# Optimization experiments

Measured on AMD Instinct MI355X. Metric: run time of the kernel, lower is better.

Reference implementation:

```python
import jax, jax.numpy as jnp
import numpy as np

B, S, D = 8, 2048, 512  # batch, seq_len, d_model (= units*heads = 64*8)


def setup_inputs() -> dict:
    key = jax.random.key(0)
    k1, k2, k3, k4 = jax.random.split(key, 4)
    scale = 1.0 / np.sqrt(D)
    return {
        "data": jax.random.normal(k1, (B, S, D), dtype=jnp.float32),
        "Wq": jax.random.normal(k2, (D, D), dtype=jnp.float32) * scale,
        "Wk": jax.random.normal(k3, (D, D), dtype=jnp.float32) * scale,
        "Wv": jax.random.normal(k4, (D, D), dtype=jnp.float32) * scale,
    }


def reference(data, Wq, Wk, Wv):
    # Bias-free projections (no head split in the original module).
    q = data @ Wq  # [B,S,D]
    k = data @ Wk
    v = data @ Wv
    scores = jnp.einsum("bsd,btd->bst", q, k)  # [B,S,S]
    # NOTE: original scales by sqrt(weight.shape[-1]) == sqrt(seq_len), not sqrt(d_k).
    scores = scores / jnp.sqrt(jnp.float32(scores.shape[-1]))
    # Causal mask: (w + 1e6) * tril - 1e6  ==  where(tril, w, -1e6)
    causal = jnp.tril(jnp.ones((scores.shape[1], scores.shape[2]), dtype=bool))
    scores = jnp.where(causal[None, :, :], scores, jnp.float32(-1e6))
    attn = jax.nn.softmax(scores, axis=-1)
    return jnp.einsum("bst,btd->bsd", attn, v)  # [B,S,D]
```

## Files before the change

### kernel.cpp

```cpp
#include <hip/hip_runtime.h>

typedef unsigned short u16;
typedef __attribute__((ext_vector_type(8))) short short8;
typedef __attribute__((ext_vector_type(4))) float f32x4;


__device__ __forceinline__ u16 f2bf(float f) {
    unsigned u = __float_as_uint(f);
    u += 0x7fffu + ((u >> 16) & 1u);
    return (u16)(u >> 16);
}

__device__ __forceinline__ void lds_cp16(const u16* g, u16* l) {
#if defined(__has_builtin) && __has_builtin(__builtin_amdgcn_global_load_lds)
    __builtin_amdgcn_global_load_lds(
        (const __attribute__((address_space(1))) void*)g,
        (__attribute__((address_space(3))) void*)l, 16, 0, 0);
#else
    *(uint4*)l = *(const uint4*)g;
#endif
}

__device__ __forceinline__ void skew(int bid) {
    const int slot = bid >> 8;
    for (int i = 0; i < slot; ++i) __builtin_amdgcn_s_sleep(7);
}

template <int MI, bool ROWSUM>
__device__ __forceinline__ void gemm64(const u16* __restrict__ Ag, int lda,
                                       const u16* __restrict__ Bg, int ldb,
                                       int ksteps, u16* Alds, u16* Blds,
                                       f32x4 (&acc)[MI][4], f32x4* accL) {
    const int t = threadIdx.x;
    const int lane = t & 63, w = t >> 6;
    const int l15 = lane & 15, g4 = lane >> 4;
    const int wr = (w >> 1) * (MI * 16);
    const int wc = (w & 1) * 64;
    const int swz = l15 & 7;
    const short ob = (short)0x3f80;
    const short8 ones = {ob, ob, ob, ob, ob, ob, ob, ob};

    for (int kt = 0; kt < ksteps; ++kt) {
        __syncthreads();
#pragma unroll
        for (int p = 0; p < MI; ++p) {
            const int gi = t + p * 256;
            const int row = gi >> 3;
            const int gl = (gi & 7) ^ (row & 7);
            lds_cp16(Ag + (size_t)row * lda + kt * 64 + gl * 8, Alds + gi * 8);
        }
#pragma unroll
        for (int p = 0; p < 4; ++p) {
            const int gi = t + p * 256;
            const int row = gi >> 3;
            const int gl = (gi & 7) ^ (row & 7);
            lds_cp16(Bg + (size_t)row * ldb + kt * 64 + gl * 8, Blds + gi * 8);
        }
        __syncthreads();
#pragma unroll
        for (int ks = 0; ks < 2; ++ks) {
            short8 a[MI], b[4];
#pragma unroll
            for (int i = 0; i < MI; ++i) {
                const int r = wr + i * 16 + l15;
                a[i] = *(const short8*)(Alds + r * 64 + (((ks * 4 + g4) ^ swz) * 8));
            }
#pragma unroll
            for (int j = 0; j < 4; ++j) {
                const int r = wc + j * 16 + l15;
                b[j] = *(const short8*)(Blds + r * 64 + (((ks * 4 + g4) ^ swz) * 8));
            }
#pragma unroll
            for (int i = 0; i < MI; ++i)
#pragma unroll
                for (int j = 0; j < 4; ++j)
                    acc[i][j] = __builtin_amdgcn_mfma_f32_16x16x32_bf16(a[i], b[j], acc[i][j], 0, 0, 0);
            if constexpr (ROWSUM) {
#pragma unroll
                for (int i = 0; i < MI; ++i)
                    accL[i] = __builtin_amdgcn_mfma_f32_16x16x32_bf16(a[i], ones, accL[i], 0, 0, 0);
            }
        }
    }
}


__global__ void k_cvt(const float4* __restrict__ X4, ushort4* __restrict__ Xb4,
                      const float* __restrict__ Wq, const float* __restrict__ Wk,
                      const float* __restrict__ Wv, u16* __restrict__ Wt) {
    const int bid = blockIdx.x, t = threadIdx.x;
    if (bid < 2048) {
        const int n4 = (8 * 2048 * 512) / 4;
        for (int i = bid * 256 + t; i < n4; i += 2048 * 256) {
            float4 v = X4[i];
            ushort4 o;
            o.x = f2bf(v.x); o.y = f2bf(v.y); o.z = f2bf(v.z); o.w = f2bf(v.w);
            Xb4[i] = o;
        }
    } else {
        const int e0 = ((bid - 2048) * 256 + t) * 4;
#pragma unroll
        for (int p = 0; p < 4; ++p) {
            const int idx = e0 + p;
            const int z = idx >> 18;
            const int rem = idx & 262143;
            float v;
            if (z == 0) v = Wq[rem];
            else if (z == 1) v = Wk[rem];
            else { int n = rem >> 9, k = rem & 511; v = Wv[k * 512 + n]; }
            Wt[idx] = f2bf(v);
        }
    }
}

__global__ __launch_bounds__(256, 4) void k_gemm_m(const u16* __restrict__ Wt, u16* __restrict__ Mt) {
    __shared__ alignas(16) u16 Alds[8192];
    __shared__ alignas(16) u16 Blds[8192];
    const int mt = blockIdx.x & 3, nt = blockIdx.x >> 2;
    const u16* Ag = Wt + 0 * 512 * 512 + (size_t)mt * 128 * 512;
    const u16* Bg = Wt + 1 * 512 * 512 + (size_t)nt * 128 * 512;
    f32x4 acc[4][4] = {};
    gemm64<4, false>(Ag, 512, Bg, 512, 8, Alds, Blds, acc, (f32x4*)nullptr);

    const int t = threadIdx.x, lane = t & 63, w = t >> 6;
    const int wr = (w >> 1) * 64, wc = (w & 1) * 64;
    const float sc = 0.022097086912079608f;
#pragma unroll
    for (int i = 0; i < 4; ++i)
#pragma unroll
        for (int j = 0; j < 4; ++j)
#pragma unroll
            for (int r = 0; r < 4; ++r) {
                int e = mt * 128 + wr + i * 16 + 4 * (lane >> 4) + r;
                int f = nt * 128 + wc + j * 16 + (lane & 15);
                Mt[(size_t)f * 512 + e] = f2bf(acc[i][j][r] * sc);
            }
}

__global__ __launch_bounds__(256, 4) void k_proj(const u16* __restrict__ Xb, const u16* __restrict__ Wt,
                                                 const u16* __restrict__ Mt,
                                                 u16* __restrict__ Gb, u16* __restrict__ Vt) {
    __shared__ alignas(16) u16 Alds[8192];
    __shared__ alignas(16) u16 Blds[8192];
    const int bid = blockIdx.x;
    const int u = bid >> 3;
    const int z = u >> 6;
    const int nt = (u >> 4) & 3;
    const int mt = (bid & 7) * 16 + (u & 15);
    const u16* Ag = Xb + (size_t)mt * 128 * 512;
    const u16* Bg = (z == 0) ? (Mt + (size_t)nt * 128 * 512)
                             : (Wt + 2 * 512 * 512 + (size_t)nt * 128 * 512);
    skew(bid);
    f32x4 acc[4][4] = {};
    gemm64<4, false>(Ag, 512, Bg, 512, 8, Alds, Blds, acc, (f32x4*)nullptr);

    const int t = threadIdx.x, lane = t & 63, w = t >> 6;
    const int wr = (w >> 1) * 64, wc = (w & 1) * 64;
    if (z == 0) {
#pragma unroll
        for (int i = 0; i < 4; ++i)
#pragma unroll
            for (int j = 0; j < 4; ++j)
#pragma unroll
                for (int r = 0; r < 4; ++r) {
                    int m = mt * 128 + wr + i * 16 + 4 * (lane >> 4) + r;
                    int n = nt * 128 + wc + j * 16 + (lane & 15);
                    Gb[(size_t)m * 512 + n] = f2bf(acc[i][j][r]);
                }
    } else {
        int b = mt >> 4;
#pragma unroll
        for (int i = 0; i < 4; ++i)
#pragma unroll
            for (int j = 0; j < 4; ++j) {
                int s0 = (mt * 128 + wr + i * 16 + 4 * (lane >> 4)) & 2047;
                int d = nt * 128 + wc + j * 16 + (lane & 15);
                ushort4 pk;
                pk.x = f2bf(acc[i][j][0]); pk.y = f2bf(acc[i][j][1]);
                pk.z = f2bf(acc[i][j][2]); pk.w = f2bf(acc[i][j][3]);
                *(ushort4*)(Vt + (size_t)b * 512 * 2048 + (size_t)d * 2048 + s0) = pk;
            }
    }
}

__global__ __launch_bounds__(256, 4) void k_scores(const u16* __restrict__ Gb, const u16* __restrict__ Xb,
                                                   u16* __restrict__ P) {
    const int bid = blockIdx.x;
    const int bz = bid & 7;
    const int tt = bid >> 3;
    int qi = (int)((sqrtf(8.0f * tt + 1.0f) - 1.0f) * 0.5f);
    while ((qi + 1) * (qi + 2) / 2 <= tt) ++qi;
    while (qi * (qi + 1) / 2 > tt) --qi;
    const int kvj = tt - qi * (qi + 1) / 2;

    __shared__ alignas(16) u16 Alds[8192];
    __shared__ alignas(16) u16 Blds[8192];
    const u16* Ag = Gb + (size_t)bz * 2048 * 512 + (size_t)qi * 128 * 512;
    const u16* Bg = Xb + (size_t)bz * 2048 * 512 + (size_t)kvj * 128 * 512;
    skew(bid);
    f32x4 acc[4][4] = {};
    gemm64<4, false>(Ag, 512, Bg, 512, 8, Alds, Blds, acc, (f32x4*)nullptr);

    const int t = threadIdx.x, lane = t & 63, w = t >> 6;
    const int wr = (w >> 1) * 64, wc = (w & 1) * 64;
    u16* Pb = P + (size_t)bz * 2048 * 2048;
#pragma unroll
    for (int i = 0; i < 4; ++i)
#pragma unroll
        for (int j = 0; j < 4; ++j)
#pragma unroll
            for (int r = 0; r < 4; ++r) {
                int q = qi * 128 + wr + i * 16 + 4 * (lane >> 4) + r;
                int kv = kvj * 128 + wc + j * 16 + (lane & 15);
                float pv = (kv <= q) ? __expf(acc[i][j][r]) : 0.0f;
                Pb[(size_t)q * 2048 + kv] = f2bf(pv);
            }
}

__global__ __launch_bounds__(256, 4) void k_pv(const u16* __restrict__ P, const u16* __restrict__ Vt,
                                               float* __restrict__ Out) {
    __shared__ alignas(16) u16 Alds[4096];
    __shared__ alignas(16) u16 Blds[8192];
    const int bid = blockIdx.x;
    const int bz = bid & 7;
    const int u = bid >> 3;
    const int g = u >> 5;
    const int s = u & 31;
    const int nt = g;
    const int qi2 = (g & 1) ? (31 - s) : s;
    const int ksteps = qi2 + 1;

    const u16* Ag = P + (size_t)bz * 2048 * 2048 + (size_t)qi2 * 64 * 2048;
    const u16* Bg = Vt + (size_t)bz * 512 * 2048 + (size_t)nt * 128 * 2048;
    skew(bid);
    f32x4 acc[2][4] = {};
    f32x4 accL[2] = {};
    gemm64<2, true>(Ag, 2048, Bg, 2048, ksteps, Alds, Blds, acc, accL);

    const int t = threadIdx.x, lane = t & 63, w = t >> 6;
    const int l = lane & 15, g4 = lane >> 4;
    const int wr = (w >> 1) * 32, wc = (w & 1) * 64;
#pragma unroll
    for (int i = 0; i < 2; ++i) {
        float inv[4];
#pragma unroll
        for (int r = 0; r < 4; ++r) inv[r] = 1.0f / accL[i][r];
#pragma unroll
        for (int j = 0; j < 4; ++j) {
            const int d = nt * 128 + wc + j * 16 + l;
#pragma unroll
            for (int r = 0; r < 4; ++r) {
                const int q = qi2 * 64 + wr + i * 16 + 4 * g4 + r;
                Out[(size_t)bz * 2048 * 512 + (size_t)q * 512 + d] = acc[i][j][r] * inv[r];
            }
        }
    }
}


extern "C" void kernel_launch(void* const* d_in, const int* in_sizes, int n_in,
                              void* d_out, int out_size, void* d_ws, size_t ws_size,
                              hipStream_t stream) {
    const float* data = (const float*)d_in[0];
    const float* Wq = (const float*)d_in[1];
    const float* Wk = (const float*)d_in[2];
    const float* Wv = (const float*)d_in[3];
    float* out = (float*)d_out;
    char* ws = (char*)d_ws;

    u16* Xb = (u16*)(ws);
    u16* Gb = (u16*)(ws + 16777216);
    u16* Mt = (u16*)(ws + 33554432);
    u16* Vt = (u16*)(ws + 50331648);
    u16* Wt = (u16*)(ws + 67108864);
    u16* P  = (u16*)(ws + 68681728);

    k_cvt<<<2816, 256, 0, stream>>>((const float4*)data, (ushort4*)Xb, Wq, Wk, Wv, Wt);
    k_gemm_m<<<16, 256, 0, stream>>>(Wt, Mt);
    k_proj<<<1024, 256, 0, stream>>>(Xb, Wt, Mt, Gb, Vt);
    k_scores<<<1088, 256, 0, stream>>>(Gb, Xb, P);
    k_pv<<<1024, 256, 0, stream>>>(P, Vt, out);
}
```

Before: 111.0 us.

## Use 512-thread blocks with larger tiles for projection, scores and PV kernels

Result: slower. 119.2 us (+7.3%).

```diff
diff --git a/kernel.cpp b/kernel.cpp
--- a/kernel.cpp
+++ b/kernel.cpp
@@ -21,11 +21,6 @@
 #endif
 }
 
-__device__ __forceinline__ void skew(int bid) {
-    const int slot = bid >> 8;
-    for (int i = 0; i < slot; ++i) __builtin_amdgcn_s_sleep(7);
-}
-
 template <int MI, bool ROWSUM>
 __device__ __forceinline__ void gemm64(const u16* __restrict__ Ag, int lda,
                                        const u16* __restrict__ Bg, int ldb,
@@ -52,6 +47,64 @@
 #pragma unroll
         for (int p = 0; p < 4; ++p) {
             const int gi = t + p * 256;
+            const int row = gi >> 3;
+            const int gl = (gi & 7) ^ (row & 7);
+            lds_cp16(Bg + (size_t)row * ldb + kt * 64 + gl * 8, Blds + gi * 8);
+        }
+        __syncthreads();
+#pragma unroll
+        for (int ks = 0; ks < 2; ++ks) {
+            short8 a[MI], b[4];
+#pragma unroll
+            for (int i = 0; i < MI; ++i) {
+                const int r = wr + i * 16 + l15;
+                a[i] = *(const short8*)(Alds + r * 64 + (((ks * 4 + g4) ^ swz) * 8));
+            }
+#pragma unroll
+            for (int j = 0; j < 4; ++j) {
+                const int r = wc + j * 16 + l15;
+                b[j] = *(const short8*)(Blds + r * 64 + (((ks * 4 + g4) ^ swz) * 8));
+            }
+#pragma unroll
+            for (int i = 0; i < MI; ++i)
+#pragma unroll
+                for (int j = 0; j < 4; ++j)
+                    acc[i][j] = __builtin_amdgcn_mfma_f32_16x16x32_bf16(a[i], b[j], acc[i][j], 0, 0, 0);
+            if constexpr (ROWSUM) {
+#pragma unroll
+                for (int i = 0; i < MI; ++i)
+                    accL[i] = __builtin_amdgcn_mfma_f32_16x16x32_bf16(a[i], ones, accL[i], 0, 0, 0);
+            }
+        }
+    }
+}
+
+template <int MI, bool ROWSUM>
+__device__ __forceinline__ void gemm512(const u16* __restrict__ Ag, int lda,
+                                        const u16* __restrict__ Bg, int ldb,
+                                        int ksteps, u16* Alds, u16* Blds,
+                                        f32x4 (&acc)[MI][4], f32x4* accL) {
+    const int t = threadIdx.x;
+    const int lane = t & 63, w = t >> 6;
+    const int l15 = lane & 15, g4 = lane >> 4;
+    const int wr = (w >> 1) * (MI * 16);
+    const int wc = (w & 1) * 64;
+    const int swz = l15 & 7;
+    const short ob = (short)0x3f80;
+    const short8 ones = {ob, ob, ob, ob, ob, ob, ob, ob};
+
+    for (int kt = 0; kt < ksteps; ++kt) {
+        __syncthreads();
+#pragma unroll
+        for (int p = 0; p < MI; ++p) {
+            const int gi = t + p * 512;
+            const int row = gi >> 3;
+            const int gl = (gi & 7) ^ (row & 7);
+            lds_cp16(Ag + (size_t)row * lda + kt * 64 + gl * 8, Alds + gi * 8);
+        }
+#pragma unroll
+        for (int p = 0; p < 2; ++p) {
+            const int gi = t + p * 512;
             const int row = gi >> 3;
             const int gl = (gi & 7) ^ (row & 7);
             lds_cp16(Bg + (size_t)row * ldb + kt * 64 + gl * 8, Blds + gi * 8);
@@ -137,24 +190,23 @@
             }
 }
 
-__global__ __launch_bounds__(256, 4) void k_proj(const u16* __restrict__ Xb, const u16* __restrict__ Wt,
+__global__ __launch_bounds__(512, 4) void k_proj(const u16* __restrict__ Xb, const u16* __restrict__ Wt,
                                                  const u16* __restrict__ Mt,
                                                  u16* __restrict__ Gb, u16* __restrict__ Vt) {
-    __shared__ alignas(16) u16 Alds[8192];
-    __shared__ alignas(16) u16 Blds[8192];
+    __shared__ alignas(16) u16 Alds[256 * 64];
+    __shared__ alignas(16) u16 Blds[128 * 64];
     const int bid = blockIdx.x;
-    const int u = bid >> 3;
-    const int z = u >> 6;
-    const int nt = (u >> 4) & 3;
-    const int mt = (bid & 7) * 16 + (u & 15);
-    const u16* Ag = Xb + (size_t)mt * 128 * 512;
+    const int mt = (bid & 7) * 8 + ((bid >> 3) & 7);
+    const int zn = bid >> 6;
+    const int z = zn >> 2, nt = zn & 3;
+    const u16* Ag = Xb + (size_t)mt * 256 * 512;
     const u16* Bg = (z == 0) ? (Mt + (size_t)nt * 128 * 512)
                              : (Wt + 2 * 512 * 512 + (size_t)nt * 128 * 512);
-    skew(bid);
     f32x4 acc[4][4] = {};
-    gemm64<4, false>(Ag, 512, Bg, 512, 8, Alds, Blds, acc, (f32x4*)nullptr);
+    gemm512<4, false>(Ag, 512, Bg, 512, 8, Alds, Blds, acc, (f32x4*)nullptr);
 
     const int t = threadIdx.x, lane = t & 63, w = t >> 6;
+    const int l15 = lane & 15, g4 = lane >> 4;
     const int wr = (w >> 1) * 64, wc = (w & 1) * 64;
     if (z == 0) {
 #pragma unroll
@@ -163,18 +215,18 @@
             for (int j = 0; j < 4; ++j)
 #pragma unroll
                 for (int r = 0; r < 4; ++r) {
-                    int m = mt * 128 + wr + i * 16 + 4 * (lane >> 4) + r;
-                    int n = nt * 128 + wc + j * 16 + (lane & 15);
+                    int m = mt * 256 + wr + i * 16 + 4 * g4 + r;
+                    int n = nt * 128 + wc + j * 16 + l15;
                     Gb[(size_t)m * 512 + n] = f2bf(acc[i][j][r]);
                 }
     } else {
-        int b = mt >> 4;
 #pragma unroll
         for (int i = 0; i < 4; ++i)
 #pragma unroll
             for (int j = 0; j < 4; ++j) {
-                int s0 = (mt * 128 + wr + i * 16 + 4 * (lane >> 4)) & 2047;
-                int d = nt * 128 + wc + j * 16 + (lane & 15);
+                int row = mt * 256 + wr + i * 16 + 4 * g4;
+                int b = row >> 11, s0 = row & 2047;
+                int d = nt * 128 + wc + j * 16 + l15;
                 ushort4 pk;
                 pk.x = f2bf(acc[i][j][0]); pk.y = f2bf(acc[i][j][1]);
                 pk.z = f2bf(acc[i][j][2]); pk.w = f2bf(acc[i][j][3]);
@@ -183,25 +235,25 @@
     }
 }
 
-__global__ __launch_bounds__(256, 4) void k_scores(const u16* __restrict__ Gb, const u16* __restrict__ Xb,
+__global__ __launch_bounds__(512, 4) void k_scores(const u16* __restrict__ Gb, const u16* __restrict__ Xb,
                                                    u16* __restrict__ P) {
+    __shared__ alignas(16) u16 Alds[256 * 64];
+    __shared__ alignas(16) u16 Blds[128 * 64];
     const int bid = blockIdx.x;
     const int bz = bid & 7;
     const int tt = bid >> 3;
-    int qi = (int)((sqrtf(8.0f * tt + 1.0f) - 1.0f) * 0.5f);
-    while ((qi + 1) * (qi + 2) / 2 <= tt) ++qi;
-    while (qi * (qi + 1) / 2 > tt) --qi;
-    const int kvj = tt - qi * (qi + 1) / 2;
-
-    __shared__ alignas(16) u16 Alds[8192];
-    __shared__ alignas(16) u16 Blds[8192];
-    const u16* Ag = Gb + (size_t)bz * 2048 * 512 + (size_t)qi * 128 * 512;
+    int qi = (int)((sqrtf(4.0f * tt + 1.0f) - 1.0f) * 0.5f);
+    while ((qi + 1) * (qi + 2) <= tt) ++qi;
+    while (qi * (qi + 1) > tt) --qi;
+    const int kvj = tt - qi * (qi + 1);
+
+    const u16* Ag = Gb + (size_t)bz * 2048 * 512 + (size_t)qi * 256 * 512;
     const u16* Bg = Xb + (size_t)bz * 2048 * 512 + (size_t)kvj * 128 * 512;
-    skew(bid);
     f32x4 acc[4][4] = {};
-    gemm64<4, false>(Ag, 512, Bg, 512, 8, Alds, Blds, acc, (f32x4*)nullptr);
+    gemm512<4, false>(Ag, 512, Bg, 512, 8, Alds, Blds, acc, (f32x4*)nullptr);
 
     const int t = threadIdx.x, lane = t & 63, w = t >> 6;
+    const int l15 = lane & 15, g4 = lane >> 4;
     const int wr = (w >> 1) * 64, wc = (w & 1) * 64;
     u16* Pb = P + (size_t)bz * 2048 * 2048;
 #pragma unroll
@@ -210,35 +262,33 @@
         for (int j = 0; j < 4; ++j)
 #pragma unroll
             for (int r = 0; r < 4; ++r) {
-                int q = qi * 128 + wr + i * 16 + 4 * (lane >> 4) + r;
-                int kv = kvj * 128 + wc + j * 16 + (lane & 15);
+                int q = qi * 256 + wr + i * 16 + 4 * g4 + r;
+                int kv = kvj * 128 + wc + j * 16 + l15;
                 float pv = (kv <= q) ? __expf(acc[i][j][r]) : 0.0f;
                 Pb[(size_t)q * 2048 + kv] = f2bf(pv);
             }
 }
 
-__global__ __launch_bounds__(256, 4) void k_pv(const u16* __restrict__ P, const u16* __restrict__ Vt,
+__global__ __launch_bounds__(512, 4) void k_pv(const u16* __restrict__ P, const u16* __restrict__ Vt,
                                                float* __restrict__ Out) {
-    __shared__ alignas(16) u16 Alds[4096];
-    __shared__ alignas(16) u16 Blds[8192];
+    __shared__ alignas(16) u16 Alds[128 * 64];
+    __shared__ alignas(16) u16 Blds[128 * 64];
     const int bid = blockIdx.x;
     const int bz = bid & 7;
-    const int u = bid >> 3;
-    const int g = u >> 5;
-    const int s = u & 31;
-    const int nt = g;
-    const int qi2 = (g & 1) ? (31 - s) : s;
-    const int ksteps = qi2 + 1;
-
-    const u16* Ag = P + (size_t)bz * 2048 * 2048 + (size_t)qi2 * 64 * 2048;
+    const int nt = (bid >> 3) & 3;
+    const int qp = (bid >> 5) & 7;
+    const int h = (bid >> 8) & 1;
+    const int qi = h ? (15 - qp) : qp;
+    const int ksteps = (qi + 1) * 2;
+
+    const u16* Ag = P + (size_t)bz * 2048 * 2048 + (size_t)qi * 128 * 2048;
     const u16* Bg = Vt + (size_t)bz * 512 * 2048 + (size_t)nt * 128 * 2048;
-    skew(bid);
     f32x4 acc[2][4] = {};
     f32x4 accL[2] = {};
-    gemm64<2, true>(Ag, 2048, Bg, 2048, ksteps, Alds, Blds, acc, accL);
+    gemm512<2, true>(Ag, 2048, Bg, 2048, ksteps, Alds, Blds, acc, accL);
 
     const int t = threadIdx.x, lane = t & 63, w = t >> 6;
-    const int l = lane & 15, g4 = lane >> 4;
+    const int l15 = lane & 15, g4 = lane >> 4;
     const int wr = (w >> 1) * 32, wc = (w & 1) * 64;
 #pragma unroll
     for (int i = 0; i < 2; ++i) {
@@ -247,10 +297,10 @@
         for (int r = 0; r < 4; ++r) inv[r] = 1.0f / accL[i][r];
 #pragma unroll
         for (int j = 0; j < 4; ++j) {
-            const int d = nt * 128 + wc + j * 16 + l;
+            const int d = nt * 128 + wc + j * 16 + l15;
 #pragma unroll
             for (int r = 0; r < 4; ++r) {
-                const int q = qi2 * 64 + wr + i * 16 + 4 * g4 + r;
+                const int q = qi * 128 + wr + i * 16 + 4 * g4 + r;
                 Out[(size_t)bz * 2048 * 512 + (size_t)q * 512 + d] = acc[i][j][r] * inv[r];
             }
         }
@@ -277,7 +327,7 @@
 
     k_cvt<<<2816, 256, 0, stream>>>((const float4*)data, (ushort4*)Xb, Wq, Wk, Wv, Wt);
     k_gemm_m<<<16, 256, 0, stream>>>(Wt, Mt);
-    k_proj<<<1024, 256, 0, stream>>>(Xb, Wt, Mt, Gb, Vt);
-    k_scores<<<1088, 256, 0, stream>>>(Gb, Xb, P);
-    k_pv<<<1024, 256, 0, stream>>>(P, Vt, out);
-}
+    k_proj<<<512, 512, 0, stream>>>(Xb, Wt, Mt, Gb, Vt);
+    k_scores<<<576, 512, 0, stream>>>(Gb, Xb, P);
+    k_pv<<<512, 512, 0, stream>>>(P, Vt, out);
+}
```
